# Kernel tuning notes

Hardware: AMD Instinct MI355X
Metric: run time of the kernel (lower is better)

The kernel has to match this reference:

```python
import jax, jax.numpy as jnp
import numpy as np
import math

DEPTH = 4
IN_FEATURES = 1024
LEAF_WIDTH = 256
OUT_FEATURES = 1024
BATCH = 8192
N_LEAVES = 2 ** DEPTH      # 16
N_NODES = 2 ** DEPTH - 1   # 15


def setup_inputs() -> dict:
    key = jax.random.key(0)
    ks = jax.random.split(key, 8)
    l1 = 1.0 / math.sqrt(IN_FEATURES)
    l2 = 1.0 / math.sqrt(LEAF_WIDTH)
    u = lambda k, shape, f: jax.random.uniform(k, shape, jnp.float32, -f, f)
    return {
        "x": jax.random.normal(ks[0], (BATCH, IN_FEATURES), jnp.float32),
        "node_weights": u(ks[1], (N_NODES, IN_FEATURES), l1),
        "node_biases": u(ks[2], (N_NODES, 1), l1),
        "w1s": u(ks[3], (N_LEAVES, IN_FEATURES, LEAF_WIDTH), l1),
        "b1s": u(ks[4], (N_LEAVES, LEAF_WIDTH), l1),
        "w2s": u(ks[5], (N_LEAVES, LEAF_WIDTH, OUT_FEATURES), l2),
        "b2s": u(ks[6], (N_LEAVES, OUT_FEATURES), l2),
    }


def reference(x, node_weights, node_biases, w1s, b1s, w2s, b2s):
    # Soft tree-gated routing (training_forward, soft decisions, no leak).
    B = x.shape[0]
    mixture = jnp.ones((B, N_LEAVES), dtype=x.dtype)
    for d in range(DEPTH):  # static small loop over tree depth
        plat, nxt = 2 ** d - 1, 2 ** (d + 1) - 1
        n = 2 ** d
        w = node_weights[plat:nxt]          # (n, F)
        b = node_biases[plat:nxt]           # (n, 1)
        logits = x @ w.T + b.T              # (B, n)
        be = jax.nn.sigmoid(logits)
        # interleave (1-be, be) along node axis -> (B, 2n, 1)
        mod = jnp.stack([1.0 - be, be], axis=-1).reshape(B, 2 * n, 1)
        mixture = (mixture.reshape(B, 2 * n, N_LEAVES // (2 * n)) * mod).reshape(B, N_LEAVES)
    # Per-leaf two-layer MLP, then mixture-weighted sum over leaves.
    h = jnp.einsum("bf,lfh->blh", x, w1s) + b1s[None]          # (B, L, H)
    a = jax.nn.relu(h)
    y = jnp.einsum("blh,lho->blo", a, w2s) + b2s[None]          # (B, L, O)
    return jnp.sum(y * mixture[:, :, None], axis=1)             # (B, O)
```

## Files before the change

### kernel.cpp

```cpp
#include <hip/hip_runtime.h>
#include <hip/hip_bf16.h>
#include <math.h>

#define BATCH 8192
#define INF   1024
#define LEAFW 256
#define OUTF  1024
#define NLEAF 16
#define NNODE 15
#define NTOT  4096
#define KEXT  4160

typedef __bf16 bf16;
typedef __bf16 bf16x4 __attribute__((ext_vector_type(4)));
typedef __bf16 bf16x8 __attribute__((ext_vector_type(8)));
typedef float  f32x4  __attribute__((ext_vector_type(4)));

#define BM 128
#define BN 128
#define BK 64

__global__ __launch_bounds__(256) void prep_weights_kernel(
    const float* __restrict__ w1, const float* __restrict__ w2,
    const float* __restrict__ b2s, bf16* __restrict__ W1T,
    bf16* __restrict__ W2T) {
  __shared__ float tile[32][33];
  int b  = blockIdx.x;
  int t  = threadIdx.x;
  int tx = t & 31, ty = t >> 5;

  if (b < 4096) {
    int l = b >> 8, rem = b & 255;
    int hb = (rem & 7) * 32, fb = (rem >> 3) * 32;
    const float* in1 = w1 + (size_t)l * INF * LEAFW;
#pragma unroll
    for (int i = 0; i < 4; ++i)
      tile[ty + 8 * i][tx] = in1[(size_t)(fb + ty + 8 * i) * LEAFW + hb + tx];
    __syncthreads();
#pragma unroll
    for (int i = 0; i < 4; ++i)
      W1T[(size_t)(l * LEAFW + hb + ty + 8 * i) * INF + fb + tx] =
          (bf16)tile[tx][ty + 8 * i];
  } else if (b < 8192) {
    int bb = b - 4096;
    int l = bb >> 8, rem = bb & 255;
    int ob = (rem & 31) * 32, hb = (rem >> 5) * 32;
    const float* in2 = w2 + (size_t)l * LEAFW * OUTF;
#pragma unroll
    for (int i = 0; i < 4; ++i)
      tile[ty + 8 * i][tx] = in2[(size_t)(hb + ty + 8 * i) * OUTF + ob + tx];
    __syncthreads();
#pragma unroll
    for (int i = 0; i < 4; ++i)
      W2T[(size_t)(ob + ty + 8 * i) * KEXT + l * LEAFW + hb + tx] =
          (bf16)tile[tx][ty + 8 * i];
  } else {
    int i = (b - 8192) * 256 + t;
    int o = i >> 6, j = i & 63;
    W2T[(size_t)o * KEXT + NTOT + j] =
        (j < NLEAF) ? (bf16)b2s[(size_t)j * OUTF + o] : (bf16)0.f;
  }
}

__global__ __launch_bounds__(256) void gating_kernel(
    const float4* __restrict__ x4, const float4* __restrict__ nw4,
    const float* __restrict__ nb, float* __restrict__ mg,
    bf16* __restrict__ Aact, bf16x4* __restrict__ Xbf4) {
  int row  = blockIdx.x * 4 + (threadIdx.x >> 6);
  int lane = threadIdx.x & 63;
  const float4* xr4 = x4 + (size_t)row * (INF / 4);

  float p[NNODE];
#pragma unroll
  for (int j = 0; j < NNODE; ++j) p[j] = 0.f;
#pragma unroll
  for (int c = 0; c < INF / 256; ++c) {
    int idx = c * 64 + lane;
    float4 xv = xr4[idx];
#pragma unroll
    for (int j = 0; j < NNODE; ++j) {
      float4 wv = nw4[j * (INF / 4) + idx];
      p[j] += xv.x * wv.x + xv.y * wv.y + xv.z * wv.z + xv.w * wv.w;
    }
    bf16x4 o = {(bf16)xv.x, (bf16)xv.y, (bf16)xv.z, (bf16)xv.w};
    Xbf4[(size_t)row * (INF / 4) + idx] = o;
  }
#pragma unroll
  for (int j = 0; j < NNODE; ++j) {
    float v = p[j];
#pragma unroll
    for (int off = 32; off > 0; off >>= 1) v += __shfl_xor(v, off);
    p[j] = 1.f / (1.f + expf(-(v + nb[j])));
  }
  float mixv[NLEAF];
#pragma unroll
  for (int L = 0; L < NLEAF; ++L) {
    int n1 = 1 + (L >> 3), n2 = 3 + (L >> 2), n3 = 7 + (L >> 1);
    float m = ((L >> 3) & 1) ? p[0] : (1.f - p[0]);
    m *= ((L >> 2) & 1) ? p[n1] : (1.f - p[n1]);
    m *= ((L >> 1) & 1) ? p[n2] : (1.f - p[n2]);
    m *= (L & 1) ? p[n3] : (1.f - p[n3]);
    mixv[L] = m;
  }
  bf16* arow = Aact + (size_t)row * KEXT + NTOT;
  if (lane == 0) {
#pragma unroll
    for (int L = 0; L < NLEAF; ++L) {
      mg[row * NLEAF + L] = mixv[L];
      arow[L] = (bf16)mixv[L];
    }
  }
  if (lane >= 16) arow[lane] = (bf16)0.f;
}

template <int EPI>
__global__ __launch_bounds__(256, 2) void gemm_kernel(
    const bf16* __restrict__ A, int lda, const bf16* __restrict__ BT, int ldb,
    int K, const float* __restrict__ bias, const float* __restrict__ mg,
    bf16* __restrict__ outB, int ldob, float* __restrict__ outF, int ldof) {
  __shared__ __align__(16) bf16 As[BM * BK];
  __shared__ __align__(16) bf16 Bs[BN * BK];

  int t    = threadIdx.x;
  int lane = t & 63;
  int w    = t >> 6;
  int bm   = blockIdx.x * BM;
  int bn   = blockIdx.y * BN;
  int wm   = (w >> 1) * 64;
  int wn   = (w & 1) * 64;

  int sr = t >> 3;
  int sc = t & 7;
  int gc = ((sc ^ (sr & 7)) << 3);

  f32x4 acc[4][4];
#pragma unroll
  for (int i = 0; i < 4; ++i)
#pragma unroll
    for (int j = 0; j < 4; ++j) acc[i][j] = (f32x4){0.f, 0.f, 0.f, 0.f};

  for (int k0 = 0; k0 < K; k0 += BK) {
#pragma unroll
    for (int i = 0; i < 4; ++i) {
      int r = i * 32 + sr;
      __builtin_amdgcn_global_load_lds(
          (const __attribute__((address_space(1))) void*)(
              A + (size_t)(bm + r) * lda + k0 + gc),
          (__attribute__((address_space(3))) void*)((char*)As + i * 4096 +
                                                    t * 16),
          16, 0, 0);
    }
#pragma unroll
    for (int i = 0; i < 4; ++i) {
      int r = i * 32 + sr;
      __builtin_amdgcn_global_load_lds(
          (const __attribute__((address_space(1))) void*)(
              BT + (size_t)(bn + r) * ldb + k0 + gc),
          (__attribute__((address_space(3))) void*)((char*)Bs + i * 4096 +
                                                    t * 16),
          16, 0, 0);
    }
    __syncthreads();

#pragma unroll
    for (int kk = 0; kk < 2; ++kk) {
      int c = (kk * 4 + (lane >> 4)) ^ (lane & 7);
      bf16x8 af[4], bfr[4];
#pragma unroll
      for (int i = 0; i < 4; ++i) {
        int R = wm + i * 16 + (lane & 15);
        af[i] = *reinterpret_cast<const bf16x8*>(&As[R * 64 + c * 8]);
      }
#pragma unroll
      for (int j = 0; j < 4; ++j) {
        int R = wn + j * 16 + (lane & 15);
        bfr[j] = *reinterpret_cast<const bf16x8*>(&Bs[R * 64 + c * 8]);
      }
#pragma unroll
      for (int i = 0; i < 4; ++i)
#pragma unroll
        for (int j = 0; j < 4; ++j)
          acc[i][j] = __builtin_amdgcn_mfma_f32_16x16x32_bf16(
              af[i], bfr[j], acc[i][j], 0, 0, 0);
    }
    __syncthreads();
  }

  int r0 = bm + wm + ((lane >> 4) << 2);
  int c0 = bn + wn + (lane & 15);
  if (EPI == 0) {
    int leaf = (bn + wn) >> 8;
#pragma unroll
    for (int i = 0; i < 4; ++i) {
#pragma unroll
      for (int r = 0; r < 4; ++r) {
        int row = r0 + i * 16 + r;
        float g = mg[row * NLEAF + leaf];
#pragma unroll
        for (int j = 0; j < 4; ++j) {
          int col = c0 + j * 16;
          float v = acc[i][j][r] + bias[col];
          v = v > 0.f ? v : 0.f;
          outB[(size_t)row * ldob + col] = (bf16)(v * g);
        }
      }
    }
  } else {
#pragma unroll
    for (int i = 0; i < 4; ++i)
#pragma unroll
      for (int r = 0; r < 4; ++r) {
        int row = r0 + i * 16 + r;
#pragma unroll
        for (int j = 0; j < 4; ++j)
          outF[(size_t)row * ldof + (c0 + j * 16)] = acc[i][j][r];
      }
  }
}

extern "C" void kernel_launch(void* const* d_in, const int* in_sizes, int n_in,
                              void* d_out, int out_size, void* d_ws,
                              size_t ws_size, hipStream_t stream) {
  const float* x   = (const float*)d_in[0];
  const float* nw  = (const float*)d_in[1];
  const float* nb  = (const float*)d_in[2];
  const float* w1s = (const float*)d_in[3];
  const float* b1s = (const float*)d_in[4];
  const float* w2s = (const float*)d_in[5];
  const float* b2s = (const float*)d_in[6];
  float* out = (float*)d_out;

  char* ws = (char*)d_ws;
  bf16*  Xbf  = (bf16*)(ws);
  bf16*  W1T  = (bf16*)(ws + 16777216);
  bf16*  W2T  = (bf16*)(ws + 25165824);
  float* mg   = (float*)(ws + 33685504);
  bf16*  Aact = (bf16*)(ws + 34209792);

  prep_weights_kernel<<<dim3(8448), 256, 0, stream>>>(w1s, w2s, b2s, W1T, W2T);
  gating_kernel<<<dim3(BATCH / 4), 256, 0, stream>>>(
      (const float4*)x, (const float4*)nw, nb, mg, Aact, (bf16x4*)Xbf);

  gemm_kernel<0><<<dim3(BATCH / BM, NTOT / BN), 256, 0, stream>>>(
      Xbf, INF, W1T, INF, INF, b1s, mg, Aact, KEXT, nullptr, 0);
  gemm_kernel<1><<<dim3(BATCH / BM, OUTF / BN), 256, 0, stream>>>(
      Aact, KEXT, W2T, KEXT, KEXT, nullptr, nullptr, nullptr, 0, out, OUTF);
}
```

Before: 285.5 us.

## Replace GEMMs with 8-wave double-buffered ping-pong kernel and larger tiles

Replaces the single-buffered 128x128 GEMM with a 512-thread kernel using 256x256 (first GEMM) and 128x256 (second GEMM) tiles. LDS is double-buffered and loads are staged in half-tiles interleaved with four MFMA phases, with explicit vmcnt waits, barriers and s_setprio. The goal is to overlap global-to-LDS traffic with MFMA work and raise arithmetic intensity per block. A swizzled block index also improves L2 reuse. The tiles use more LDS and registers per block, which risks lower occupancy, and correctness depends on the hand-tuned waitcnt counts.

```diff
diff --git a/kernel.cpp b/kernel.cpp
--- a/kernel.cpp
+++ b/kernel.cpp
@@ -16,10 +16,6 @@
 typedef __bf16 bf16x8 __attribute__((ext_vector_type(8)));
 typedef float  f32x4  __attribute__((ext_vector_type(4)));
 
-#define BM 128
-#define BN 128
-#define BK 64
-
 __global__ __launch_bounds__(256) void prep_weights_kernel(
     const float* __restrict__ w1, const float* __restrict__ w2,
     const float* __restrict__ b2s, bf16* __restrict__ W1T,
@@ -113,108 +109,194 @@
   if (lane >= 16) arow[lane] = (bf16)0.f;
 }
 
-template <int EPI>
-__global__ __launch_bounds__(256, 2) void gemm_kernel(
+
+template <int N>
+__device__ __forceinline__ void wait_vmcnt() {
+  if constexpr (N >= 0) {
+    asm volatile("s_waitcnt vmcnt(%0)" ::"n"(N) : "memory");
+  }
+}
+
+#define GEMM_PHASE(PM, PN, STAGE_STMT, VM)                                     \
+  do {                                                                         \
+    bf16x8 af[FM / 2][2], bq[2][2];                                            \
+    _Pragma("unroll") for (int ii = 0; ii < FM / 2; ++ii) {                    \
+      _Pragma("unroll") for (int kk = 0; kk < 2; ++kk) {                       \
+        af[ii][kk] = rdA(cur, (PM) * (FM / 2) + ii, kk);                       \
+      }                                                                        \
+    }                                                                          \
+    _Pragma("unroll") for (int jj = 0; jj < 2; ++jj) {                         \
+      _Pragma("unroll") for (int kk = 0; kk < 2; ++kk) {                       \
+        bq[jj][kk] = rdB(cur, (PN) * 2 + jj, kk);                              \
+      }                                                                        \
+    }                                                                          \
+    STAGE_STMT;                                                                \
+    asm volatile("" ::: "memory");                                             \
+    __builtin_amdgcn_s_barrier();                                              \
+    asm volatile("s_waitcnt lgkmcnt(0)" ::: "memory");                         \
+    __builtin_amdgcn_s_setprio(1);                                             \
+    _Pragma("unroll") for (int kk = 0; kk < 2; ++kk) {                         \
+      _Pragma("unroll") for (int ii = 0; ii < FM / 2; ++ii) {                  \
+        _Pragma("unroll") for (int jj = 0; jj < 2; ++jj) {                     \
+          acc[(PM) * (FM / 2) + ii][(PN) * 2 + jj] =                           \
+              __builtin_amdgcn_mfma_f32_16x16x32_bf16(                         \
+                  af[ii][kk], bq[jj][kk],                                      \
+                  acc[(PM) * (FM / 2) + ii][(PN) * 2 + jj], 0, 0, 0);          \
+        }                                                                      \
+      }                                                                        \
+    }                                                                          \
+    __builtin_amdgcn_s_setprio(0);                                             \
+    wait_vmcnt<(VM)>();                                                        \
+    asm volatile("" ::: "memory");                                             \
+    __builtin_amdgcn_s_barrier();                                              \
+    asm volatile("" ::: "memory");                                             \
+  } while (0)
+
+template <int TBM, int EPI>
+__global__ __launch_bounds__(512, 2) void gemm8_kernel(
     const bf16* __restrict__ A, int lda, const bf16* __restrict__ BT, int ldb,
     int K, const float* __restrict__ bias, const float* __restrict__ mg,
-    bf16* __restrict__ outB, int ldob, float* __restrict__ outF, int ldof) {
-  __shared__ __align__(16) bf16 As[BM * BK];
-  __shared__ __align__(16) bf16 Bs[BN * BK];
-
-  int t    = threadIdx.x;
-  int lane = t & 63;
-  int w    = t >> 6;
-  int bm   = blockIdx.x * BM;
-  int bn   = blockIdx.y * BN;
-  int wm   = (w >> 1) * 64;
-  int wn   = (w & 1) * 64;
-
-  int sr = t >> 3;
-  int sc = t & 7;
-  int gc = ((sc ^ (sr & 7)) << 3);
-
-  f32x4 acc[4][4];
-#pragma unroll
-  for (int i = 0; i < 4; ++i)
-#pragma unroll
-    for (int j = 0; j < 4; ++j) acc[i][j] = (f32x4){0.f, 0.f, 0.f, 0.f};
-
-  for (int k0 = 0; k0 < K; k0 += BK) {
-#pragma unroll
-    for (int i = 0; i < 4; ++i) {
-      int r = i * 32 + sr;
+    bf16* __restrict__ outB, int ldob, float* __restrict__ outF, int ldof,
+    int ntn) {
+  static_assert(TBM == 256 || TBM == 128, "TBM");
+  constexpr int HHA = TBM / 2;
+  constexpr int LA  = TBM / 128;
+  constexpr int LB  = 2;
+  constexpr int FM  = TBM / 32;
+  constexpr int FN  = 4;
+  constexpr int ASZ = TBM * 64;
+  constexpr int BSZ = 256 * 64;
+  constexpr int VM1 = 2 * LA + 2 * LB;
+  constexpr int VM2 = LA + 2 * LB;
+
+  __shared__ __align__(16) bf16 As[2 * ASZ];
+  __shared__ __align__(16) bf16 Bs[2 * BSZ];
+
+  const int t    = threadIdx.x;
+  const int lane = t & 63;
+  const int w    = t >> 6;
+  const int wm   = w >> 2;
+  const int wn   = w & 3;
+
+  const int nwg  = gridDim.x;
+  const int orig = blockIdx.x;
+  const int swz  = (orig & 7) * (nwg >> 3) + (orig >> 3);
+  const int bm   = (swz / ntn) * TBM;
+  const int bn   = (swz % ntn) * 256;
+
+  const int lr   = t >> 3;
+  const int cs   = t & 7;
+  const int scol = ((cs ^ (lr & 7)) << 3);
+
+  auto stageA = [&](int kt, int h, int buf) {
+#pragma unroll
+    for (int q = 0; q < LA; ++q) {
+      const bf16* src =
+          A + (size_t)(bm + h * HHA + q * 64 + lr) * lda + kt * 64 + scol;
       __builtin_amdgcn_global_load_lds(
-          (const __attribute__((address_space(1))) void*)(
-              A + (size_t)(bm + r) * lda + k0 + gc),
-          (__attribute__((address_space(3))) void*)((char*)As + i * 4096 +
+          (const __attribute__((address_space(1))) void*)src,
+          (__attribute__((address_space(3))) void*)((char*)As +
+                                                    buf * (ASZ * 2) +
+                                                    h * (HHA * 128) +
+                                                    q * 8192 + t * 16),
+          16, 0, 0);
+    }
+  };
+  auto stageB = [&](int kt, int h, int buf) {
+#pragma unroll
+    for (int q = 0; q < LB; ++q) {
+      const bf16* src =
+          BT + (size_t)(bn + h * 128 + q * 64 + lr) * ldb + kt * 64 + scol;
+      __builtin_amdgcn_global_load_lds(
+          (const __attribute__((address_space(1))) void*)src,
+          (__attribute__((address_space(3))) void*)((char*)Bs +
+                                                    buf * (BSZ * 2) +
+                                                    h * 16384 + q * 8192 +
                                                     t * 16),
           16, 0, 0);
     }
-#pragma unroll
-    for (int i = 0; i < 4; ++i) {
-      int r = i * 32 + sr;
-      __builtin_amdgcn_global_load_lds(
-          (const __attribute__((address_space(1))) void*)(
-              BT + (size_t)(bn + r) * ldb + k0 + gc),
-          (__attribute__((address_space(3))) void*)((char*)Bs + i * 4096 +
-                                                    t * 16),
-          16, 0, 0);
-    }
-    __syncthreads();
-
-#pragma unroll
-    for (int kk = 0; kk < 2; ++kk) {
-      int c = (kk * 4 + (lane >> 4)) ^ (lane & 7);
-      bf16x8 af[4], bfr[4];
-#pragma unroll
-      for (int i = 0; i < 4; ++i) {
-        int R = wm + i * 16 + (lane & 15);
-        af[i] = *reinterpret_cast<const bf16x8*>(&As[R * 64 + c * 8]);
-      }
-#pragma unroll
-      for (int j = 0; j < 4; ++j) {
-        int R = wn + j * 16 + (lane & 15);
-        bfr[j] = *reinterpret_cast<const bf16x8*>(&Bs[R * 64 + c * 8]);
-      }
-#pragma unroll
-      for (int i = 0; i < 4; ++i)
-#pragma unroll
-        for (int j = 0; j < 4; ++j)
-          acc[i][j] = __builtin_amdgcn_mfma_f32_16x16x32_bf16(
-              af[i], bfr[j], acc[i][j], 0, 0, 0);
-    }
-    __syncthreads();
-  }
-
-  int r0 = bm + wm + ((lane >> 4) << 2);
-  int c0 = bn + wn + (lane & 15);
-  if (EPI == 0) {
-    int leaf = (bn + wn) >> 8;
-#pragma unroll
-    for (int i = 0; i < 4; ++i) {
-#pragma unroll
-      for (int r = 0; r < 4; ++r) {
-        int row = r0 + i * 16 + r;
-        float g = mg[row * NLEAF + leaf];
-#pragma unroll
-        for (int j = 0; j < 4; ++j) {
-          int col = c0 + j * 16;
-          float v = acc[i][j][r] + bias[col];
+  };
+  auto rdA = [&](int buf, int i, int kk) -> bf16x8 {
+    int h, r;
+    if constexpr (TBM == 256) {
+      h = i >> 2;
+      r = wm * 64 + (i & 3) * 16 + (lane & 15);
+    } else {
+      h = i >> 1;
+      r = wm * 32 + (i & 1) * 16 + (lane & 15);
+    }
+    int ch = ((kk << 2) + (lane >> 4)) ^ (lane & 7);
+    return *reinterpret_cast<const bf16x8*>(
+        &As[buf * ASZ + h * (HHA * 64) + r * 64 + ch * 8]);
+  };
+  auto rdB = [&](int buf, int j, int kk) -> bf16x8 {
+    int h = j >> 1;
+    int r = wn * 32 + (j & 1) * 16 + (lane & 15);
+    int ch = ((kk << 2) + (lane >> 4)) ^ (lane & 7);
+    return *reinterpret_cast<const bf16x8*>(
+        &Bs[buf * BSZ + h * 8192 + r * 64 + ch * 8]);
+  };
+
+  f32x4 acc[FM][FN];
+#pragma unroll
+  for (int i = 0; i < FM; ++i)
+#pragma unroll
+    for (int j = 0; j < FN; ++j) acc[i][j] = (f32x4){0.f, 0.f, 0.f, 0.f};
+
+  const int NT = K >> 6;
+
+  stageB(0, 0, 0);
+  stageA(0, 1, 0);
+  stageA(0, 0, 0);
+  stageB(0, 1, 0);
+  const int k1p = NT > 1 ? 1 : 0;
+  stageB(k1p, 0, 1);
+  stageA(k1p, 1, 1);
+  wait_vmcnt<VM2>();
+  asm volatile("" ::: "memory");
+  __builtin_amdgcn_s_barrier();
+  asm volatile("" ::: "memory");
+
+  for (int kt = 0; kt < NT; ++kt) {
+    const int cur = kt & 1, nxt = cur ^ 1;
+    const int k1 = kt + 1 < NT ? kt + 1 : NT - 1;
+    const int k2 = kt + 2 < NT ? kt + 2 : NT - 1;
+    GEMM_PHASE(0, 0, stageA(k1, 0, nxt), -1);
+    GEMM_PHASE(1, 0, stageB(k1, 1, nxt), VM1);
+    GEMM_PHASE(1, 1, stageB(k2, 0, cur), -1);
+    GEMM_PHASE(0, 1, stageA(k2, 1, cur), VM2);
+  }
+
+#pragma unroll
+  for (int i = 0; i < FM; ++i) {
+    int rb;
+    if constexpr (TBM == 256)
+      rb = (i >> 2) * 128 + wm * 64 + (i & 3) * 16;
+    else
+      rb = (i >> 1) * 64 + wm * 32 + (i & 1) * 16;
+    rb += bm + ((lane >> 4) << 2);
+#pragma unroll
+    for (int rr = 0; rr < 4; ++rr) {
+      const int grow = rb + rr;
+      if constexpr (EPI == 0) {
+        const float g = mg[grow * NLEAF + (bn >> 8)];
+#pragma unroll
+        for (int j = 0; j < FN; ++j) {
+          const int gcol =
+              bn + (j >> 1) * 128 + wn * 32 + (j & 1) * 16 + (lane & 15);
+          float v = acc[i][j][rr] + bias[gcol];
           v = v > 0.f ? v : 0.f;
-          outB[(size_t)row * ldob + col] = (bf16)(v * g);
+          outB[(size_t)grow * ldob + gcol] = (bf16)(v * g);
+        }
+      } else {
+#pragma unroll
+        for (int j = 0; j < FN; ++j) {
+          const int gcol =
+              bn + (j >> 1) * 128 + wn * 32 + (j & 1) * 16 + (lane & 15);
+          outF[(size_t)grow * ldof + gcol] = acc[i][j][rr];
         }
       }
     }
-  } else {
-#pragma unroll
-    for (int i = 0; i < 4; ++i)
-#pragma unroll
-      for (int r = 0; r < 4; ++r) {
-        int row = r0 + i * 16 + r;
-#pragma unroll
-        for (int j = 0; j < 4; ++j)
-          outF[(size_t)row * ldof + (c0 + j * 16)] = acc[i][j][r];
-      }
   }
 }
 
@@ -241,8 +323,9 @@
   gating_kernel<<<dim3(BATCH / 4), 256, 0, stream>>>(
       (const float4*)x, (const float4*)nw, nb, mg, Aact, (bf16x4*)Xbf);
 
-  gemm_kernel<0><<<dim3(BATCH / BM, NTOT / BN), 256, 0, stream>>>(
-      Xbf, INF, W1T, INF, INF, b1s, mg, Aact, KEXT, nullptr, 0);
-  gemm_kernel<1><<<dim3(BATCH / BM, OUTF / BN), 256, 0, stream>>>(
-      Aact, KEXT, W2T, KEXT, KEXT, nullptr, nullptr, nullptr, 0, out, OUTF);
-}
+  gemm8_kernel<256, 0><<<dim3((BATCH / 256) * (NTOT / 256)), 512, 0, stream>>>(
+      Xbf, INF, W1T, INF, INF, b1s, mg, Aact, KEXT, nullptr, 0, NTOT / 256);
+  gemm8_kernel<128, 1><<<dim3((BATCH / 128) * (OUTF / 256)), 512, 0, stream>>>(
+      Aact, KEXT, W2T, KEXT, KEXT, nullptr, nullptr, nullptr, 0, out, OUTF,
+      OUTF / 256);
+}
```

After: 317.9 us. +11.4%, slower.

## Rewrite GEMMs with larger tiles, double-buffered LDS and split-phase pipelining

Applied to the files above, without the earlier changes.

Replaces the generic 128x128 single-buffered GEMM with two specialized kernels that use 512-thread blocks, 256x256 (GEMM1) and 128x256 (GEMM2) tiles, and double-buffered LDS. Loads for the next K step are issued in quarters between MFMA phases, ordered with explicit vmcnt waits and raw barriers, and MFMA phases run at raised wave priority. A block-index swizzle is added to improve L2 locality. The aim is to hide global-to-LDS latency and raise arithmetic intensity per tile, at the cost of more LDS and registers, which may limit occupancy, and of fragile hand-ordered synchronization.

```diff
diff --git a/kernel.cpp b/kernel.cpp
--- a/kernel.cpp
+++ b/kernel.cpp
@@ -16,10 +16,6 @@
 typedef __bf16 bf16x8 __attribute__((ext_vector_type(8)));
 typedef float  f32x4  __attribute__((ext_vector_type(4)));
 
-#define BM 128
-#define BN 128
-#define BK 64
-
 __global__ __launch_bounds__(256) void prep_weights_kernel(
     const float* __restrict__ w1, const float* __restrict__ w2,
     const float* __restrict__ b2s, bf16* __restrict__ W1T,
@@ -113,108 +109,315 @@
   if (lane >= 16) arow[lane] = (bf16)0.f;
 }
 
-template <int EPI>
-__global__ __launch_bounds__(256, 2) void gemm_kernel(
-    const bf16* __restrict__ A, int lda, const bf16* __restrict__ BT, int ldb,
-    int K, const float* __restrict__ bias, const float* __restrict__ mg,
-    bf16* __restrict__ outB, int ldob, float* __restrict__ outF, int ldof) {
-  __shared__ __align__(16) bf16 As[BM * BK];
-  __shared__ __align__(16) bf16 Bs[BN * BK];
-
-  int t    = threadIdx.x;
-  int lane = t & 63;
-  int w    = t >> 6;
-  int bm   = blockIdx.x * BM;
-  int bn   = blockIdx.y * BN;
-  int wm   = (w >> 1) * 64;
-  int wn   = (w & 1) * 64;
-
-  int sr = t >> 3;
-  int sc = t & 7;
-  int gc = ((sc ^ (sr & 7)) << 3);
-
-  f32x4 acc[4][4];
-#pragma unroll
-  for (int i = 0; i < 4; ++i)
-#pragma unroll
-    for (int j = 0; j < 4; ++j) acc[i][j] = (f32x4){0.f, 0.f, 0.f, 0.f};
-
-  for (int k0 = 0; k0 < K; k0 += BK) {
-#pragma unroll
-    for (int i = 0; i < 4; ++i) {
-      int r = i * 32 + sr;
+template <int N>
+__device__ __forceinline__ void wait_vmcnt() {
+  asm volatile("s_waitcnt vmcnt(%0)" ::"n"(N) : "memory");
+}
+__device__ __forceinline__ void barrier_fence() {
+  asm volatile("" ::: "memory");
+  __builtin_amdgcn_s_barrier();
+  asm volatile("" ::: "memory");
+}
+
+__global__ __launch_bounds__(512, 2) void gemm1_kernel(
+    const bf16* __restrict__ A, const bf16* __restrict__ BT,
+    const float* __restrict__ bias, const float* __restrict__ mg,
+    bf16* __restrict__ outB) {
+  constexpr int NT  = INF / 64;
+  constexpr int ASZ = 256 * 64;
+  constexpr int BSZ = 256 * 64;
+  __shared__ __align__(16) bf16 As[2 * ASZ];
+  __shared__ __align__(16) bf16 Bs[2 * BSZ];
+
+  const int t = threadIdx.x, lane = t & 63, w = t >> 6;
+  const int wm = w >> 2, wn = w & 3;
+  const int orig = blockIdx.x;
+  const int swz  = (orig & 7) * 64 + (orig >> 3);
+  const int bm = (swz >> 4) * 256, bn = (swz & 15) * 256;
+  const int lr = t >> 3, cs = t & 7;
+  const int scol = ((cs ^ (lr & 7)) << 3);
+
+  auto stageA = [&](int kt, int h, int buf) {
+#pragma unroll
+    for (int q = 0; q < 2; ++q) {
+      const bf16* src =
+          A + (size_t)(bm + h * 128 + q * 64 + lr) * INF + kt * 64 + scol;
       __builtin_amdgcn_global_load_lds(
-          (const __attribute__((address_space(1))) void*)(
-              A + (size_t)(bm + r) * lda + k0 + gc),
-          (__attribute__((address_space(3))) void*)((char*)As + i * 4096 +
+          (const __attribute__((address_space(1))) void*)src,
+          (__attribute__((address_space(3))) void*)((char*)As +
+                                                    buf * (ASZ * 2) +
+                                                    h * 16384 + q * 8192 +
                                                     t * 16),
           16, 0, 0);
     }
-#pragma unroll
-    for (int i = 0; i < 4; ++i) {
-      int r = i * 32 + sr;
+  };
+  auto stageB = [&](int kt, int h, int buf) {
+#pragma unroll
+    for (int q = 0; q < 2; ++q) {
+      const bf16* src =
+          BT + (size_t)(bn + h * 128 + q * 64 + lr) * INF + kt * 64 + scol;
       __builtin_amdgcn_global_load_lds(
-          (const __attribute__((address_space(1))) void*)(
-              BT + (size_t)(bn + r) * ldb + k0 + gc),
-          (__attribute__((address_space(3))) void*)((char*)Bs + i * 4096 +
+          (const __attribute__((address_space(1))) void*)src,
+          (__attribute__((address_space(3))) void*)((char*)Bs +
+                                                    buf * (BSZ * 2) +
+                                                    h * 16384 + q * 8192 +
                                                     t * 16),
           16, 0, 0);
     }
-    __syncthreads();
-
-#pragma unroll
-    for (int kk = 0; kk < 2; ++kk) {
-      int c = (kk * 4 + (lane >> 4)) ^ (lane & 7);
-      bf16x8 af[4], bfr[4];
-#pragma unroll
-      for (int i = 0; i < 4; ++i) {
-        int R = wm + i * 16 + (lane & 15);
-        af[i] = *reinterpret_cast<const bf16x8*>(&As[R * 64 + c * 8]);
+  };
+  auto rdA = [&](int buf, int i, int kk) -> bf16x8 {
+    int r  = wm * 64 + (i & 3) * 16 + (lane & 15);
+    int ch = ((kk << 2) + (lane >> 4)) ^ (lane & 7);
+    return *reinterpret_cast<const bf16x8*>(
+        &As[buf * ASZ + (i >> 2) * 8192 + r * 64 + ch * 8]);
+  };
+  auto rdB = [&](int buf, int j, int kk) -> bf16x8 {
+    int r  = wn * 32 + (j & 1) * 16 + (lane & 15);
+    int ch = ((kk << 2) + (lane >> 4)) ^ (lane & 7);
+    return *reinterpret_cast<const bf16x8*>(
+        &Bs[buf * BSZ + (j >> 1) * 8192 + r * 64 + ch * 8]);
+  };
+
+  f32x4 acc[8][4];
+#pragma unroll
+  for (int i = 0; i < 8; ++i)
+#pragma unroll
+    for (int j = 0; j < 4; ++j) acc[i][j] = (f32x4){0.f, 0.f, 0.f, 0.f};
+
+  stageA(0, 0, 0);
+  stageB(0, 0, 0);
+  stageB(0, 1, 0);
+  stageA(0, 1, 0);
+  wait_vmcnt<4>();
+  barrier_fence();
+
+  for (int kt = 0; kt < NT; ++kt) {
+    const int cur = kt & 1, nxt = cur ^ 1;
+    const int k1 = kt + 1 < NT ? kt + 1 : NT - 1;
+    bf16x8 af0[4][2], af1[4][2], bq0[2][2], bq1[2][2];
+
+#pragma unroll
+    for (int i = 0; i < 4; ++i)
+#pragma unroll
+      for (int kk = 0; kk < 2; ++kk) af0[i][kk] = rdA(cur, i, kk);
+#pragma unroll
+    for (int j = 0; j < 2; ++j)
+#pragma unroll
+      for (int kk = 0; kk < 2; ++kk) bq0[j][kk] = rdB(cur, j, kk);
+    stageA(k1, 0, nxt);
+    __builtin_amdgcn_s_setprio(1);
+#pragma unroll
+    for (int kk = 0; kk < 2; ++kk)
+#pragma unroll
+      for (int i = 0; i < 4; ++i)
+#pragma unroll
+        for (int j = 0; j < 2; ++j)
+          acc[i][j] = __builtin_amdgcn_mfma_f32_16x16x32_bf16(
+              af0[i][kk], bq0[j][kk], acc[i][j], 0, 0, 0);
+    __builtin_amdgcn_s_setprio(0);
+    wait_vmcnt<4>();
+    barrier_fence();
+
+#pragma unroll
+    for (int j = 0; j < 2; ++j)
+#pragma unroll
+      for (int kk = 0; kk < 2; ++kk) bq1[j][kk] = rdB(cur, 2 + j, kk);
+    stageB(k1, 0, nxt);
+    __builtin_amdgcn_s_setprio(1);
+#pragma unroll
+    for (int kk = 0; kk < 2; ++kk)
+#pragma unroll
+      for (int i = 0; i < 4; ++i)
+#pragma unroll
+        for (int j = 0; j < 2; ++j)
+          acc[i][2 + j] = __builtin_amdgcn_mfma_f32_16x16x32_bf16(
+              af0[i][kk], bq1[j][kk], acc[i][2 + j], 0, 0, 0);
+    __builtin_amdgcn_s_setprio(0);
+    wait_vmcnt<4>();
+    barrier_fence();
+
+#pragma unroll
+    for (int i = 0; i < 4; ++i)
+#pragma unroll
+      for (int kk = 0; kk < 2; ++kk) af1[i][kk] = rdA(cur, 4 + i, kk);
+    stageB(k1, 1, nxt);
+    __builtin_amdgcn_s_setprio(1);
+#pragma unroll
+    for (int kk = 0; kk < 2; ++kk)
+#pragma unroll
+      for (int i = 0; i < 4; ++i)
+#pragma unroll
+        for (int j = 0; j < 2; ++j)
+          acc[4 + i][2 + j] = __builtin_amdgcn_mfma_f32_16x16x32_bf16(
+              af1[i][kk], bq1[j][kk], acc[4 + i][2 + j], 0, 0, 0);
+    __builtin_amdgcn_s_setprio(0);
+    wait_vmcnt<6>();
+    barrier_fence();
+
+    stageA(k1, 1, nxt);
+    __builtin_amdgcn_s_setprio(1);
+#pragma unroll
+    for (int kk = 0; kk < 2; ++kk)
+#pragma unroll
+      for (int i = 0; i < 4; ++i)
+#pragma unroll
+        for (int j = 0; j < 2; ++j)
+          acc[4 + i][j] = __builtin_amdgcn_mfma_f32_16x16x32_bf16(
+              af1[i][kk], bq0[j][kk], acc[4 + i][j], 0, 0, 0);
+    __builtin_amdgcn_s_setprio(0);
+    wait_vmcnt<4>();
+    barrier_fence();
+  }
+
+  const int leaf = bn >> 8;
+#pragma unroll
+  for (int i = 0; i < 8; ++i) {
+    int rb = bm + (i >> 2) * 128 + wm * 64 + (i & 3) * 16 + ((lane >> 4) << 2);
+#pragma unroll
+    for (int rr = 0; rr < 4; ++rr) {
+      const int grow = rb + rr;
+      const float g  = mg[grow * NLEAF + leaf];
+#pragma unroll
+      for (int j = 0; j < 4; ++j) {
+        const int gcol =
+            bn + (j >> 1) * 128 + wn * 32 + (j & 1) * 16 + (lane & 15);
+        float v = acc[i][j][rr] + bias[gcol];
+        v = v > 0.f ? v : 0.f;
+        outB[(size_t)grow * KEXT + gcol] = (bf16)(v * g);
       }
+    }
+  }
+}
+
+__global__ __launch_bounds__(512, 2) void gemm2_kernel(
+    const bf16* __restrict__ A, const bf16* __restrict__ BT,
+    float* __restrict__ outF) {
+  constexpr int NT  = KEXT / 64;
+  constexpr int ASZ = 128 * 64;
+  constexpr int BSZ = 256 * 64;
+  __shared__ __align__(16) bf16 As[2 * ASZ];
+  __shared__ __align__(16) bf16 Bs[2 * BSZ];
+
+  const int t = threadIdx.x, lane = t & 63, w = t >> 6;
+  const int wm = w >> 2, wn = w & 3;
+  const int orig = blockIdx.x;
+  const int swz  = (orig & 7) * 32 + (orig >> 3);
+  const int bm = (swz >> 2) * 128, bn = (swz & 3) * 256;
+  const int lr = t >> 3, cs = t & 7;
+  const int scol = ((cs ^ (lr & 7)) << 3);
+
+  auto stageA = [&](int kt, int buf) {
+#pragma unroll
+    for (int q = 0; q < 2; ++q) {
+      const bf16* src =
+          A + (size_t)(bm + q * 64 + lr) * KEXT + kt * 64 + scol;
+      __builtin_amdgcn_global_load_lds(
+          (const __attribute__((address_space(1))) void*)src,
+          (__attribute__((address_space(3))) void*)((char*)As +
+                                                    buf * (ASZ * 2) +
+                                                    q * 8192 + t * 16),
+          16, 0, 0);
+    }
+  };
+  auto stageB = [&](int kt, int h, int buf) {
+#pragma unroll
+    for (int q = 0; q < 2; ++q) {
+      const bf16* src =
+          BT + (size_t)(bn + h * 128 + q * 64 + lr) * KEXT + kt * 64 + scol;
+      __builtin_amdgcn_global_load_lds(
+          (const __attribute__((address_space(1))) void*)src,
+          (__attribute__((address_space(3))) void*)((char*)Bs +
+                                                    buf * (BSZ * 2) +
+                                                    h * 16384 + q * 8192 +
+                                                    t * 16),
+          16, 0, 0);
+    }
+  };
+  auto rdA = [&](int buf, int i, int kk) -> bf16x8 {
+    int r  = (i >> 1) * 64 + wm * 32 + (i & 1) * 16 + (lane & 15);
+    int ch = ((kk << 2) + (lane >> 4)) ^ (lane & 7);
+    return *reinterpret_cast<const bf16x8*>(
+        &As[buf * ASZ + r * 64 + ch * 8]);
+  };
+  auto rdB = [&](int buf, int j, int kk) -> bf16x8 {
+    int r  = wn * 32 + (j & 1) * 16 + (lane & 15);
+    int ch = ((kk << 2) + (lane >> 4)) ^ (lane & 7);
+    return *reinterpret_cast<const bf16x8*>(
+        &Bs[buf * BSZ + (j >> 1) * 8192 + r * 64 + ch * 8]);
+  };
+
+  f32x4 acc[4][4];
+#pragma unroll
+  for (int i = 0; i < 4; ++i)
+#pragma unroll
+    for (int j = 0; j < 4; ++j) acc[i][j] = (f32x4){0.f, 0.f, 0.f, 0.f};
+
+  stageA(0, 0);
+  stageB(0, 0, 0);
+  stageB(0, 1, 0);
+  wait_vmcnt<2>();
+  barrier_fence();
+
+  for (int kt = 0; kt < NT; ++kt) {
+    const int cur = kt & 1, nxt = cur ^ 1;
+    const int k1 = kt + 1 < NT ? kt + 1 : NT - 1;
+    bf16x8 af[4][2], bq0[2][2], bq1[2][2];
+
+#pragma unroll
+    for (int i = 0; i < 4; ++i)
+#pragma unroll
+      for (int kk = 0; kk < 2; ++kk) af[i][kk] = rdA(cur, i, kk);
+#pragma unroll
+    for (int j = 0; j < 2; ++j)
+#pragma unroll
+      for (int kk = 0; kk < 2; ++kk) bq0[j][kk] = rdB(cur, j, kk);
+    stageA(k1, nxt);
+    stageB(k1, 0, nxt);
+    __builtin_amdgcn_s_setprio(1);
+#pragma unroll
+    for (int kk = 0; kk < 2; ++kk)
+#pragma unroll
+      for (int i = 0; i < 4; ++i)
+#pragma unroll
+        for (int j = 0; j < 2; ++j)
+          acc[i][j] = __builtin_amdgcn_mfma_f32_16x16x32_bf16(
+              af[i][kk], bq0[j][kk], acc[i][j], 0, 0, 0);
+    __builtin_amdgcn_s_setprio(0);
+    wait_vmcnt<4>();
+    barrier_fence();
+
+#pragma unroll
+    for (int j = 0; j < 2; ++j)
+#pragma unroll
+      for (int kk = 0; kk < 2; ++kk) bq1[j][kk] = rdB(cur, 2 + j, kk);
+    stageB(k1, 1, nxt);
+    __builtin_amdgcn_s_setprio(1);
+#pragma unroll
+    for (int kk = 0; kk < 2; ++kk)
+#pragma unroll
+      for (int i = 0; i < 4; ++i)
+#pragma unroll
+        for (int j = 0; j < 2; ++j)
+          acc[i][2 + j] = __builtin_amdgcn_mfma_f32_16x16x32_bf16(
+              af[i][kk], bq1[j][kk], acc[i][2 + j], 0, 0, 0);
+    __builtin_amdgcn_s_setprio(0);
+    wait_vmcnt<2>();
+    barrier_fence();
+  }
+
+#pragma unroll
+  for (int i = 0; i < 4; ++i) {
+    int rb = bm + (i >> 1) * 64 + wm * 32 + (i & 1) * 16 + ((lane >> 4) << 2);
+#pragma unroll
+    for (int rr = 0; rr < 4; ++rr) {
+      const int grow = rb + rr;
 #pragma unroll
       for (int j = 0; j < 4; ++j) {
-        int R = wn + j * 16 + (lane & 15);
-        bfr[j] = *reinterpret_cast<const bf16x8*>(&Bs[R * 64 + c * 8]);
+        const int gcol =
+            bn + (j >> 1) * 128 + wn * 32 + (j & 1) * 16 + (lane & 15);
+        outF[(size_t)grow * OUTF + gcol] = acc[i][j][rr];
       }
-#pragma unroll
-      for (int i = 0; i < 4; ++i)
-#pragma unroll
-        for (int j = 0; j < 4; ++j)
-          acc[i][j] = __builtin_amdgcn_mfma_f32_16x16x32_bf16(
-              af[i], bfr[j], acc[i][j], 0, 0, 0);
-    }
-    __syncthreads();
-  }
-
-  int r0 = bm + wm + ((lane >> 4) << 2);
-  int c0 = bn + wn + (lane & 15);
-  if (EPI == 0) {
-    int leaf = (bn + wn) >> 8;
-#pragma unroll
-    for (int i = 0; i < 4; ++i) {
-#pragma unroll
-      for (int r = 0; r < 4; ++r) {
-        int row = r0 + i * 16 + r;
-        float g = mg[row * NLEAF + leaf];
-#pragma unroll
-        for (int j = 0; j < 4; ++j) {
-          int col = c0 + j * 16;
-          float v = acc[i][j][r] + bias[col];
-          v = v > 0.f ? v : 0.f;
-          outB[(size_t)row * ldob + col] = (bf16)(v * g);
-        }
-      }
-    }
-  } else {
-#pragma unroll
-    for (int i = 0; i < 4; ++i)
-#pragma unroll
-      for (int r = 0; r < 4; ++r) {
-        int row = r0 + i * 16 + r;
-#pragma unroll
-        for (int j = 0; j < 4; ++j)
-          outF[(size_t)row * ldof + (c0 + j * 16)] = acc[i][j][r];
-      }
+    }
   }
 }
 
@@ -241,8 +444,6 @@
   gating_kernel<<<dim3(BATCH / 4), 256, 0, stream>>>(
       (const float4*)x, (const float4*)nw, nb, mg, Aact, (bf16x4*)Xbf);
 
-  gemm_kernel<0><<<dim3(BATCH / BM, NTOT / BN), 256, 0, stream>>>(
-      Xbf, INF, W1T, INF, INF, b1s, mg, Aact, KEXT, nullptr, 0);
-  gemm_kernel<1><<<dim3(BATCH / BM, OUTF / BN), 256, 0, stream>>>(
-      Aact, KEXT, W2T, KEXT, KEXT, nullptr, nullptr, nullptr, 0, out, OUTF);
-}
+  gemm1_kernel<<<dim3(512), 512, 0, stream>>>(Xbf, W1T, b1s, mg, Aact);
+  gemm2_kernel<<<dim3(256), 512, 0, stream>>>(Aact, W2T, out);
+}
```

New measurement: 267.3 us. 1.07x faster.

## Double-buffer GEMM with larger 128x256 tiles, block swizzle, and fused prep kernel

Applied to the files above, without the earlier changes.

Rewrites the bf16 MFMA GEMM to use 512-thread blocks with 128x256 output tiles and double-buffered LDS. The next K-tile is prefetched via global_load_lds while the current one feeds the MFMAs, with manual vmcnt waits, s_setprio, and a block-index swizzle for L2 locality. It also merges the weight-prep and gating kernels into a single launch. The goal is to hide global-load latency, cut barrier stalls and launch overhead, and raise arithmetic intensity, at the cost of more LDS (96KB per block), which may limit occupancy. The second GEMM runs only 256 blocks, which may underfill the GPU.

```diff
diff --git a/kernel.cpp b/kernel.cpp
--- a/kernel.cpp
+++ b/kernel.cpp
@@ -16,58 +16,56 @@
 typedef __bf16 bf16x8 __attribute__((ext_vector_type(8)));
 typedef float  f32x4  __attribute__((ext_vector_type(4)));
 
-#define BM 128
-#define BN 128
-#define BK 64
-
-__global__ __launch_bounds__(256) void prep_weights_kernel(
+__global__ __launch_bounds__(256) void prep_gating_kernel(
     const float* __restrict__ w1, const float* __restrict__ w2,
-    const float* __restrict__ b2s, bf16* __restrict__ W1T,
-    bf16* __restrict__ W2T) {
+    const float* __restrict__ b2s, const float4* __restrict__ x4,
+    const float4* __restrict__ nw4, const float* __restrict__ nb,
+    bf16* __restrict__ W1T, bf16* __restrict__ W2T, float* __restrict__ mg,
+    bf16* __restrict__ Aact, bf16x4* __restrict__ Xbf4) {
   __shared__ float tile[32][33];
-  int b  = blockIdx.x;
-  int t  = threadIdx.x;
-  int tx = t & 31, ty = t >> 5;
-
-  if (b < 4096) {
-    int l = b >> 8, rem = b & 255;
-    int hb = (rem & 7) * 32, fb = (rem >> 3) * 32;
-    const float* in1 = w1 + (size_t)l * INF * LEAFW;
-#pragma unroll
-    for (int i = 0; i < 4; ++i)
-      tile[ty + 8 * i][tx] = in1[(size_t)(fb + ty + 8 * i) * LEAFW + hb + tx];
-    __syncthreads();
-#pragma unroll
-    for (int i = 0; i < 4; ++i)
-      W1T[(size_t)(l * LEAFW + hb + ty + 8 * i) * INF + fb + tx] =
-          (bf16)tile[tx][ty + 8 * i];
-  } else if (b < 8192) {
-    int bb = b - 4096;
-    int l = bb >> 8, rem = bb & 255;
-    int ob = (rem & 31) * 32, hb = (rem >> 5) * 32;
-    const float* in2 = w2 + (size_t)l * LEAFW * OUTF;
-#pragma unroll
-    for (int i = 0; i < 4; ++i)
-      tile[ty + 8 * i][tx] = in2[(size_t)(hb + ty + 8 * i) * OUTF + ob + tx];
-    __syncthreads();
-#pragma unroll
-    for (int i = 0; i < 4; ++i)
-      W2T[(size_t)(ob + ty + 8 * i) * KEXT + l * LEAFW + hb + tx] =
-          (bf16)tile[tx][ty + 8 * i];
-  } else {
-    int i = (b - 8192) * 256 + t;
-    int o = i >> 6, j = i & 63;
-    W2T[(size_t)o * KEXT + NTOT + j] =
-        (j < NLEAF) ? (bf16)b2s[(size_t)j * OUTF + o] : (bf16)0.f;
-  }
-}
-
-__global__ __launch_bounds__(256) void gating_kernel(
-    const float4* __restrict__ x4, const float4* __restrict__ nw4,
-    const float* __restrict__ nb, float* __restrict__ mg,
-    bf16* __restrict__ Aact, bf16x4* __restrict__ Xbf4) {
-  int row  = blockIdx.x * 4 + (threadIdx.x >> 6);
-  int lane = threadIdx.x & 63;
+  int b = blockIdx.x;
+  int t = threadIdx.x;
+
+  if (b < 8448) {
+    int tx = t & 31, ty = t >> 5;
+    if (b < 4096) {
+      int l = b >> 8, rem = b & 255;
+      int hb = (rem & 7) * 32, fb = (rem >> 3) * 32;
+      const float* in1 = w1 + (size_t)l * INF * LEAFW;
+#pragma unroll
+      for (int i = 0; i < 4; ++i)
+        tile[ty + 8 * i][tx] =
+            in1[(size_t)(fb + ty + 8 * i) * LEAFW + hb + tx];
+      __syncthreads();
+#pragma unroll
+      for (int i = 0; i < 4; ++i)
+        W1T[(size_t)(l * LEAFW + hb + ty + 8 * i) * INF + fb + tx] =
+            (bf16)tile[tx][ty + 8 * i];
+    } else if (b < 8192) {
+      int bb = b - 4096;
+      int l = bb >> 8, rem = bb & 255;
+      int ob = (rem & 31) * 32, hb = (rem >> 5) * 32;
+      const float* in2 = w2 + (size_t)l * LEAFW * OUTF;
+#pragma unroll
+      for (int i = 0; i < 4; ++i)
+        tile[ty + 8 * i][tx] =
+            in2[(size_t)(hb + ty + 8 * i) * OUTF + ob + tx];
+      __syncthreads();
+#pragma unroll
+      for (int i = 0; i < 4; ++i)
+        W2T[(size_t)(ob + ty + 8 * i) * KEXT + l * LEAFW + hb + tx] =
+            (bf16)tile[tx][ty + 8 * i];
+    } else {
+      int i = (b - 8192) * 256 + t;
+      int o = i >> 6, j = i & 63;
+      W2T[(size_t)o * KEXT + NTOT + j] =
+          (j < NLEAF) ? (bf16)b2s[(size_t)j * OUTF + o] : (bf16)0.f;
+    }
+    return;
+  }
+
+  int row  = (b - 8448) * 4 + (t >> 6);
+  int lane = t & 63;
   const float4* xr4 = x4 + (size_t)row * (INF / 4);
 
   float p[NNODE];
@@ -113,108 +111,158 @@
   if (lane >= 16) arow[lane] = (bf16)0.f;
 }
 
-template <int EPI>
-__global__ __launch_bounds__(256, 2) void gemm_kernel(
-    const bf16* __restrict__ A, int lda, const bf16* __restrict__ BT, int ldb,
-    int K, const float* __restrict__ bias, const float* __restrict__ mg,
-    bf16* __restrict__ outB, int ldob, float* __restrict__ outF, int ldof) {
-  __shared__ __align__(16) bf16 As[BM * BK];
-  __shared__ __align__(16) bf16 Bs[BN * BK];
-
-  int t    = threadIdx.x;
-  int lane = t & 63;
-  int w    = t >> 6;
-  int bm   = blockIdx.x * BM;
-  int bn   = blockIdx.y * BN;
-  int wm   = (w >> 1) * 64;
-  int wn   = (w & 1) * 64;
-
-  int sr = t >> 3;
-  int sc = t & 7;
-  int gc = ((sc ^ (sr & 7)) << 3);
-
-  f32x4 acc[4][4];
-#pragma unroll
-  for (int i = 0; i < 4; ++i)
-#pragma unroll
-    for (int j = 0; j < 4; ++j) acc[i][j] = (f32x4){0.f, 0.f, 0.f, 0.f};
-
-  for (int k0 = 0; k0 < K; k0 += BK) {
-#pragma unroll
-    for (int i = 0; i < 4; ++i) {
-      int r = i * 32 + sr;
+template <int N>
+__device__ __forceinline__ void wait_vmcnt() {
+  asm volatile("s_waitcnt vmcnt(%0)" ::"n"(N) : "memory");
+}
+__device__ __forceinline__ void barrier_fence() {
+  asm volatile("" ::: "memory");
+  __builtin_amdgcn_s_barrier();
+  asm volatile("" ::: "memory");
+}
+
+template <int EPI, int KLD, int NTN>
+__global__ __launch_bounds__(512, 2) void gemm_kernel(
+    const bf16* __restrict__ A, const bf16* __restrict__ BT,
+    const float* __restrict__ bias, const float* __restrict__ mg,
+    bf16* __restrict__ outB, float* __restrict__ outF) {
+  constexpr int NT  = KLD / 64;
+  constexpr int ASZ = 128 * 64;
+  constexpr int BSZ = 256 * 64;
+  __shared__ __align__(16) bf16 As[2 * ASZ];
+  __shared__ __align__(16) bf16 Bs[2 * BSZ];
+
+  const int t = threadIdx.x, lane = t & 63, w = t >> 6;
+  const int wm = w >> 2, wn = w & 3;
+  const int orig = blockIdx.x;
+  const int swz  = (orig & 7) * (8 * NTN) + (orig >> 3);
+  const int bm = (swz / NTN) * 128, bn = (swz % NTN) * 256;
+  const int lr = t >> 3, cs = t & 7;
+  const int scol = ((cs ^ (lr & 7)) << 3);
+
+  auto stageA = [&](int kt, int buf) {
+#pragma unroll
+    for (int q = 0; q < 2; ++q) {
+      const bf16* src = A + (size_t)(bm + q * 64 + lr) * KLD + kt * 64 + scol;
       __builtin_amdgcn_global_load_lds(
-          (const __attribute__((address_space(1))) void*)(
-              A + (size_t)(bm + r) * lda + k0 + gc),
-          (__attribute__((address_space(3))) void*)((char*)As + i * 4096 +
+          (const __attribute__((address_space(1))) void*)src,
+          (__attribute__((address_space(3))) void*)((char*)As +
+                                                    buf * (ASZ * 2) +
+                                                    q * 8192 + t * 16),
+          16, 0, 0);
+    }
+  };
+  auto stageB = [&](int kt, int h, int buf) {
+#pragma unroll
+    for (int q = 0; q < 2; ++q) {
+      const bf16* src =
+          BT + (size_t)(bn + h * 128 + q * 64 + lr) * KLD + kt * 64 + scol;
+      __builtin_amdgcn_global_load_lds(
+          (const __attribute__((address_space(1))) void*)src,
+          (__attribute__((address_space(3))) void*)((char*)Bs +
+                                                    buf * (BSZ * 2) +
+                                                    h * 16384 + q * 8192 +
                                                     t * 16),
           16, 0, 0);
     }
-#pragma unroll
-    for (int i = 0; i < 4; ++i) {
-      int r = i * 32 + sr;
-      __builtin_amdgcn_global_load_lds(
-          (const __attribute__((address_space(1))) void*)(
-              BT + (size_t)(bn + r) * ldb + k0 + gc),
-          (__attribute__((address_space(3))) void*)((char*)Bs + i * 4096 +
-                                                    t * 16),
-          16, 0, 0);
-    }
-    __syncthreads();
-
-#pragma unroll
-    for (int kk = 0; kk < 2; ++kk) {
-      int c = (kk * 4 + (lane >> 4)) ^ (lane & 7);
-      bf16x8 af[4], bfr[4];
-#pragma unroll
-      for (int i = 0; i < 4; ++i) {
-        int R = wm + i * 16 + (lane & 15);
-        af[i] = *reinterpret_cast<const bf16x8*>(&As[R * 64 + c * 8]);
-      }
-#pragma unroll
-      for (int j = 0; j < 4; ++j) {
-        int R = wn + j * 16 + (lane & 15);
-        bfr[j] = *reinterpret_cast<const bf16x8*>(&Bs[R * 64 + c * 8]);
-      }
-#pragma unroll
-      for (int i = 0; i < 4; ++i)
-#pragma unroll
-        for (int j = 0; j < 4; ++j)
+  };
+  auto rdA = [&](int buf, int i, int kk) -> bf16x8 {
+    int r  = (i >> 1) * 64 + wm * 32 + (i & 1) * 16 + (lane & 15);
+    int ch = ((kk << 2) + (lane >> 4)) ^ (lane & 7);
+    return *reinterpret_cast<const bf16x8*>(
+        &As[buf * ASZ + r * 64 + ch * 8]);
+  };
+  auto rdB = [&](int buf, int j, int kk) -> bf16x8 {
+    int r  = wn * 32 + (j & 1) * 16 + (lane & 15);
+    int ch = ((kk << 2) + (lane >> 4)) ^ (lane & 7);
+    return *reinterpret_cast<const bf16x8*>(
+        &Bs[buf * BSZ + (j >> 1) * 8192 + r * 64 + ch * 8]);
+  };
+
+  f32x4 acc[4][4];
+#pragma unroll
+  for (int i = 0; i < 4; ++i)
+#pragma unroll
+    for (int j = 0; j < 4; ++j) acc[i][j] = (f32x4){0.f, 0.f, 0.f, 0.f};
+
+  stageA(0, 0);
+  stageB(0, 0, 0);
+  stageB(0, 1, 0);
+  wait_vmcnt<2>();
+  barrier_fence();
+
+  for (int kt = 0; kt < NT; ++kt) {
+    const int cur = kt & 1, nxt = cur ^ 1;
+    const int k1 = kt + 1 < NT ? kt + 1 : NT - 1;
+    bf16x8 af[4][2], bq0[2][2], bq1[2][2];
+
+#pragma unroll
+    for (int i = 0; i < 4; ++i)
+#pragma unroll
+      for (int kk = 0; kk < 2; ++kk) af[i][kk] = rdA(cur, i, kk);
+#pragma unroll
+    for (int j = 0; j < 2; ++j)
+#pragma unroll
+      for (int kk = 0; kk < 2; ++kk) bq0[j][kk] = rdB(cur, j, kk);
+    stageA(k1, nxt);
+    stageB(k1, 0, nxt);
+    __builtin_amdgcn_s_setprio(1);
+#pragma unroll
+    for (int kk = 0; kk < 2; ++kk)
+#pragma unroll
+      for (int i = 0; i < 4; ++i)
+#pragma unroll
+        for (int j = 0; j < 2; ++j)
           acc[i][j] = __builtin_amdgcn_mfma_f32_16x16x32_bf16(
-              af[i], bfr[j], acc[i][j], 0, 0, 0);
-    }
-    __syncthreads();
-  }
-
-  int r0 = bm + wm + ((lane >> 4) << 2);
-  int c0 = bn + wn + (lane & 15);
-  if (EPI == 0) {
-    int leaf = (bn + wn) >> 8;
-#pragma unroll
-    for (int i = 0; i < 4; ++i) {
-#pragma unroll
-      for (int r = 0; r < 4; ++r) {
-        int row = r0 + i * 16 + r;
-        float g = mg[row * NLEAF + leaf];
+              af[i][kk], bq0[j][kk], acc[i][j], 0, 0, 0);
+    __builtin_amdgcn_s_setprio(0);
+    wait_vmcnt<4>();
+    barrier_fence();
+
+#pragma unroll
+    for (int j = 0; j < 2; ++j)
+#pragma unroll
+      for (int kk = 0; kk < 2; ++kk) bq1[j][kk] = rdB(cur, 2 + j, kk);
+    stageB(k1, 1, nxt);
+    __builtin_amdgcn_s_setprio(1);
+#pragma unroll
+    for (int kk = 0; kk < 2; ++kk)
+#pragma unroll
+      for (int i = 0; i < 4; ++i)
+#pragma unroll
+        for (int j = 0; j < 2; ++j)
+          acc[i][2 + j] = __builtin_amdgcn_mfma_f32_16x16x32_bf16(
+              af[i][kk], bq1[j][kk], acc[i][2 + j], 0, 0, 0);
+    __builtin_amdgcn_s_setprio(0);
+    wait_vmcnt<2>();
+    barrier_fence();
+  }
+
+#pragma unroll
+  for (int i = 0; i < 4; ++i) {
+    int rb = bm + (i >> 1) * 64 + wm * 32 + (i & 1) * 16 + ((lane >> 4) << 2);
+#pragma unroll
+    for (int rr = 0; rr < 4; ++rr) {
+      const int grow = rb + rr;
+      if constexpr (EPI == 0) {
+        const float g = mg[grow * NLEAF + (bn >> 8)];
 #pragma unroll
         for (int j = 0; j < 4; ++j) {
-          int col = c0 + j * 16;
-          float v = acc[i][j][r] + bias[col];
+          const int gcol =
+              bn + (j >> 1) * 128 + wn * 32 + (j & 1) * 16 + (lane & 15);
+          float v = acc[i][j][rr] + bias[gcol];
           v = v > 0.f ? v : 0.f;
-          outB[(size_t)row * ldob + col] = (bf16)(v * g);
+          outB[(size_t)grow * KEXT + gcol] = (bf16)(v * g);
+        }
+      } else {
+#pragma unroll
+        for (int j = 0; j < 4; ++j) {
+          const int gcol =
+              bn + (j >> 1) * 128 + wn * 32 + (j & 1) * 16 + (lane & 15);
+          outF[(size_t)grow * OUTF + gcol] = acc[i][j][rr];
         }
       }
     }
-  } else {
-#pragma unroll
-    for (int i = 0; i < 4; ++i)
-#pragma unroll
-      for (int r = 0; r < 4; ++r) {
-        int row = r0 + i * 16 + r;
-#pragma unroll
-        for (int j = 0; j < 4; ++j)
-          outF[(size_t)row * ldof + (c0 + j * 16)] = acc[i][j][r];
-      }
   }
 }
 
@@ -237,12 +285,12 @@
   float* mg   = (float*)(ws + 33685504);
   bf16*  Aact = (bf16*)(ws + 34209792);
 
-  prep_weights_kernel<<<dim3(8448), 256, 0, stream>>>(w1s, w2s, b2s, W1T, W2T);
-  gating_kernel<<<dim3(BATCH / 4), 256, 0, stream>>>(
-      (const float4*)x, (const float4*)nw, nb, mg, Aact, (bf16x4*)Xbf);
-
-  gemm_kernel<0><<<dim3(BATCH / BM, NTOT / BN), 256, 0, stream>>>(
-      Xbf, INF, W1T, INF, INF, b1s, mg, Aact, KEXT, nullptr, 0);
-  gemm_kernel<1><<<dim3(BATCH / BM, OUTF / BN), 256, 0, stream>>>(
-      Aact, KEXT, W2T, KEXT, KEXT, nullptr, nullptr, nullptr, 0, out, OUTF);
-}
+  prep_gating_kernel<<<dim3(10496), 256, 0, stream>>>(
+      w1s, w2s, b2s, (const float4*)x, (const float4*)nw, nb, W1T, W2T, mg,
+      Aact, (bf16x4*)Xbf);
+
+  gemm_kernel<0, INF, 16><<<dim3(1024), 512, 0, stream>>>(
+      Xbf, W1T, b1s, mg, Aact, nullptr);
+  gemm_kernel<1, KEXT, 4><<<dim3(256), 512, 0, stream>>>(
+      Aact, W2T, nullptr, nullptr, nullptr, out);
+}
```

Result: faster. 268.2 us (-6.1%).
